# Kernel tuning notes

Measured on AMD Instinct MI355X. Metric: run time of the kernel, lower is better.

## Reference

```python
import jax, jax.numpy as jnp
import numpy as np

N_NODES = 50000
N_EDGES = 800000
IN_DIM = 6
HID = 256
OUT = 256
N_EXPERTS = 8
N_LAYERS = 2
N_GRAPHS = 64


def setup_inputs() -> dict:
    key = jax.random.key(0)
    ks = jax.random.split(key, 16)
    s = 0.05
    x = jax.random.normal(ks[0], (N_NODES, IN_DIM), dtype=jnp.float32)
    edge_index = jax.random.randint(ks[1], (2, N_EDGES), 0, N_NODES, dtype=jnp.int64)
    batch = jnp.sort(jax.random.randint(ks[2], (N_NODES,), 0, N_GRAPHS, dtype=jnp.int64))
    # shared encoder
    W_enc = jax.random.normal(ks[3], (IN_DIM, HID), jnp.float32) * s
    b_enc = jnp.zeros((HID,), jnp.float32)
    # router MLP: (HID+2) -> HID -> N_EXPERTS
    Wr1 = jax.random.normal(ks[4], (HID + 2, HID), jnp.float32) * s
    br1 = jnp.zeros((HID,), jnp.float32)
    Wr2 = jax.random.normal(ks[5], (HID, N_EXPERTS), jnp.float32) * s
    br2 = jnp.zeros((N_EXPERTS,), jnp.float32)
    # experts: 2 GraphConv layers each (self weight + neighbor weight + bias), stacked over experts
    Ws0 = jax.random.normal(ks[6], (N_EXPERTS, HID, HID), jnp.float32) * s
    Wn0 = jax.random.normal(ks[7], (N_EXPERTS, HID, HID), jnp.float32) * s
    b0 = jnp.zeros((N_EXPERTS, HID), jnp.float32)
    Ws1 = jax.random.normal(ks[8], (N_EXPERTS, HID, OUT), jnp.float32) * s
    Wn1 = jax.random.normal(ks[9], (N_EXPERTS, HID, OUT), jnp.float32) * s
    b1 = jnp.zeros((N_EXPERTS, OUT), jnp.float32)
    return dict(x=x, edge_index=edge_index, batch=batch, W_enc=W_enc, b_enc=b_enc,
                Wr1=Wr1, br1=br1, Wr2=Wr2, br2=br2,
                Ws0=Ws0, Wn0=Wn0, b0=b0, Ws1=Ws1, Wn1=Wn1, b1=b1)


def _graph_conv(h, src, dst, Ws, Wn, b):
    # PyG GraphConv: x' = x @ Ws + sum_{j in N(i)} x_j @ Wn + b
    msg = h[src] @ Wn                                   # [E, d_out]
    agg = jax.ops.segment_sum(msg, dst, num_segments=N_NODES)
    return h @ Ws + agg + b


def reference(x, edge_index, batch, W_enc, b_enc, Wr1, br1, Wr2, br2,
              Ws0, Wn0, b0, Ws1, Wn1, b1):
    src, dst = edge_index[0], edge_index[1]
    # shared encoder
    h = jax.nn.relu(x @ W_enc + b_enc)                  # [N, HID]
    # graph size features: per-graph node count and edge count, log-scaled, broadcast to nodes
    ones_n = jnp.ones((h.shape[0],), h.dtype)
    node_cnt = jax.ops.segment_sum(ones_n, batch, num_segments=N_GRAPHS)
    edge_cnt = jax.ops.segment_sum(jnp.ones((src.shape[0],), h.dtype), batch[src], num_segments=N_GRAPHS)
    size_feat = jnp.stack([jnp.log1p(node_cnt)[batch], jnp.log1p(edge_cnt)[batch]], axis=-1)  # [N, 2]
    # router -> top-1 expert index
    r = jax.nn.relu(jnp.concatenate([h, size_feat], axis=-1) @ Wr1 + br1)
    logits = r @ Wr2 + br2                              # [N, n_experts]
    idx = jnp.argmax(logits, axis=-1)                   # [N]
    # dense compute-all-experts, then gather by argmax (faithful to original)
    out = jnp.zeros((h.shape[0], Ws1.shape[-1]), h.dtype)
    for e in range(N_EXPERTS):
        z = jax.nn.relu(_graph_conv(h, src, dst, Ws0[e], Wn0[e], b0[e]))
        y_e = _graph_conv(z, src, dst, Ws1[e], Wn1[e], b1[e])   # [N, OUT]
        out = out + jnp.where((idx == e)[:, None], y_e, 0.0)
    return out
```

## Files before the change

### kernel.cpp

```cpp
#include <hip/hip_runtime.h>
#include <hip/hip_bf16.h>
#include <math.h>

#define NN 50000
#define NE 800000
#define NG 64
#define NEXP 8
#define ZC_CAP (3 * NN)

typedef __attribute__((ext_vector_type(8))) short bf16x8;
typedef __attribute__((ext_vector_type(4))) float f32x4;
typedef unsigned short ushort_t;

__device__ __forceinline__ unsigned short f2bf(float f) {
  union { float f; unsigned u; } x; x.f = f;
  unsigned r = x.u + 0x7fff + ((x.u >> 16) & 1);
  return (unsigned short)(r >> 16);
}
__device__ __forceinline__ float bf2f(unsigned short u) {
  union { unsigned u; float f; } x; x.u = ((unsigned)u) << 16; return x.f;
}

__device__ __forceinline__ void gld16(const void* g, void* l) {
  __builtin_amdgcn_global_load_lds(
      (const __attribute__((address_space(1))) unsigned int*)g,
      (__attribute__((address_space(3))) unsigned int*)l, 16, 0, 0);
}

__global__ __launch_bounds__(256) void k_encoder(
    const float* __restrict__ x, const float* __restrict__ W,
    const float* __restrict__ b, ushort_t* __restrict__ Xb,
    ushort_t* __restrict__ Xlo) {
  int i = blockIdx.x, n = threadIdx.x;
  float acc = b[n];
#pragma unroll
  for (int k = 0; k < 6; k++) acc = fmaf(x[i * 6 + k], W[k * 256 + n], acc);
  acc = fmaxf(acc, 0.f);
  unsigned short hb = f2bf(acc);
  Xb[(size_t)i * 512 + n] = hb;
  Xlo[(size_t)i * 256 + n] = f2bf(acc - bf2f(hb));
}

__global__ __launch_bounds__(256) void k_count_nodes(
    const int* __restrict__ batch, int* __restrict__ node_cnt) {
  __shared__ int bins[NG];
  int t = threadIdx.x;
  if (t < NG) bins[t] = 0;
  __syncthreads();
  for (int i = blockIdx.x * blockDim.x + t; i < NN; i += gridDim.x * blockDim.x)
    atomicAdd(&bins[batch[i]], 1);
  __syncthreads();
  if (t < NG) atomicAdd(&node_cnt[t], bins[t]);
}

__global__ __launch_bounds__(256) void k_count_edges(
    const int* __restrict__ ei, const int* __restrict__ batch,
    int* __restrict__ edge_cnt, int* __restrict__ deg) {
  __shared__ int bins[NG];
  int t = threadIdx.x;
  if (t < NG) bins[t] = 0;
  __syncthreads();
  for (int e = blockIdx.x * blockDim.x + t; e < NE; e += gridDim.x * blockDim.x) {
    int s = ei[e];
    int d = ei[NE + e];
    atomicAdd(&bins[batch[s]], 1);
    atomicAdd(&deg[d], 1);
  }
  __syncthreads();
  if (t < NG) atomicAdd(&edge_cnt[t], bins[t]);
}

__global__ __launch_bounds__(256) void k_sizefeat(
    const int* __restrict__ batch, const int* __restrict__ node_cnt,
    const int* __restrict__ edge_cnt, float* __restrict__ sf0,
    float* __restrict__ sf1) {
  int i = blockIdx.x * blockDim.x + threadIdx.x;
  if (i < NN) {
    int g = batch[i];
    sf0[i] = log1pf((float)node_cnt[g]);
    sf1[i] = log1pf((float)edge_cnt[g]);
  }
}

__global__ __launch_bounds__(1024) void k_scan(
    const int* __restrict__ deg, int* __restrict__ offs, int* __restrict__ cursor) {
  __shared__ int wsums[16];
  int t = threadIdx.x, lane = t & 63, wid = t >> 6;
  int carry = 0;
  for (int base = 0; base < NN; base += 1024) {
    int i = base + t;
    int v = (i < NN) ? deg[i] : 0;
    int x = v;
#pragma unroll
    for (int d = 1; d < 64; d <<= 1) {
      int y = __shfl_up(x, d, 64);
      if (lane >= d) x += y;
    }
    if (lane == 63) wsums[wid] = x;
    __syncthreads();
    if (wid == 0) {
      int s = (lane < 16) ? wsums[lane] : 0;
#pragma unroll
      for (int d = 1; d < 16; d <<= 1) {
        int y = __shfl_up(s, d, 64);
        if (lane >= d) s += y;
      }
      if (lane < 16) wsums[lane] = s;
    }
    __syncthreads();
    int wpre = (wid > 0) ? wsums[wid - 1] : 0;
    int excl = carry + wpre + x - v;
    if (i < NN) { offs[i] = excl; cursor[i] = excl; }
    int btot = wsums[15];
    __syncthreads();
    carry += btot;
  }
  if (t == 0) offs[NN] = carry;
}

__global__ __launch_bounds__(256) void k_fill_csr(
    const int* __restrict__ ei, int* __restrict__ cursor, int* __restrict__ edge_src) {
  int e = blockIdx.x * blockDim.x + threadIdx.x;
  if (e < NE) {
    int d = ei[NE + e];
    int pos = atomicAdd(&cursor[d], 1);
    edge_src[pos] = ei[e];
  }
}

__global__ __launch_bounds__(256) void k_agg_h2(
    const int* __restrict__ offs, const int* __restrict__ edge_src,
    ushort_t* __restrict__ Xb) {
  int wid = threadIdx.x >> 6, lane = threadIdx.x & 63;
  int half = lane >> 5, cl = lane & 31;
  int i = blockIdx.x * 4 + wid;
  if (i >= NN) return;
  int e0 = offs[i], e1 = offs[i + 1];
  float acc[8] = {};
  int k = e0;
  for (; k + 8 <= e1; k += 8) {
    int s0 = edge_src[k + half];
    int s1 = edge_src[k + 2 + half];
    int s2 = edge_src[k + 4 + half];
    int s3 = edge_src[k + 6 + half];
    bf16x8 v0 = *(const bf16x8*)&Xb[(size_t)s0 * 512 + cl * 8];
    bf16x8 v1 = *(const bf16x8*)&Xb[(size_t)s1 * 512 + cl * 8];
    bf16x8 v2 = *(const bf16x8*)&Xb[(size_t)s2 * 512 + cl * 8];
    bf16x8 v3 = *(const bf16x8*)&Xb[(size_t)s3 * 512 + cl * 8];
#pragma unroll
    for (int j = 0; j < 8; j++) acc[j] += bf2f((unsigned short)v0[j]);
#pragma unroll
    for (int j = 0; j < 8; j++) acc[j] += bf2f((unsigned short)v1[j]);
#pragma unroll
    for (int j = 0; j < 8; j++) acc[j] += bf2f((unsigned short)v2[j]);
#pragma unroll
    for (int j = 0; j < 8; j++) acc[j] += bf2f((unsigned short)v3[j]);
  }
  for (; k + 2 <= e1; k += 2) {
    int s0 = edge_src[k + half];
    bf16x8 v0 = *(const bf16x8*)&Xb[(size_t)s0 * 512 + cl * 8];
#pragma unroll
    for (int j = 0; j < 8; j++) acc[j] += bf2f((unsigned short)v0[j]);
  }
  if (k < e1 && half == 0) {
    int s0 = edge_src[k];
    bf16x8 v0 = *(const bf16x8*)&Xb[(size_t)s0 * 512 + cl * 8];
#pragma unroll
    for (int j = 0; j < 8; j++) acc[j] += bf2f((unsigned short)v0[j]);
  }
#pragma unroll
  for (int j = 0; j < 8; j++) acc[j] += __shfl_xor(acc[j], 32, 64);
  if (half == 0) {
    bf16x8 o;
#pragma unroll
    for (int j = 0; j < 8; j++) o[j] = (short)f2bf(acc[j]);
    *(bf16x8*)(&Xb[(size_t)i * 512 + 256 + cl * 8]) = o;
  }
}

__global__ __launch_bounds__(256) void k_prep_w(
    const float* __restrict__ Ws0, const float* __restrict__ Wn0,
    const float* __restrict__ Ws1, const float* __restrict__ Wn1,
    ushort_t* __restrict__ Wt1, ushort_t* __restrict__ Wt2) {
  __shared__ float tile[32][33];
  int z = blockIdx.z;
  int e = z & 7;
  const float* Ws = (z < 8) ? Ws0 : Ws1;
  const float* Wn = (z < 8) ? Wn0 : Wn1;
  ushort_t* Wt = (z < 8) ? Wt1 : Wt2;
  int kt = blockIdx.x;
  int nt = blockIdx.y;
  int tx = threadIdx.x & 31, ty = threadIdx.x >> 5;
  const float* src = (kt < 8) ? (Ws + e * 65536 + (kt * 32) * 256)
                              : (Wn + e * 65536 + ((kt - 8) * 32) * 256);
#pragma unroll
  for (int rr = 0; rr < 32; rr += 8) {
    int k = rr + ty;
    tile[k][tx] = src[k * 256 + nt * 32 + tx];
  }
  __syncthreads();
#pragma unroll
  for (int rr = 0; rr < 32; rr += 8) {
    int n = rr + ty;
    Wt[(size_t)e * 131072 + (nt * 32 + n) * 512 + kt * 32 + tx] = f2bf(tile[tx][n]);
  }
}

__global__ __launch_bounds__(256) void k_prep_wr1(
    const float* __restrict__ Wr1, ushort_t* __restrict__ Wr1t) {
  int k = blockIdx.x;
  int n = threadIdx.x;
  unsigned short v;
  if (k < 256) {
    v = f2bf(Wr1[k * 256 + n]);
  } else {
    float f = Wr1[(k - 256) * 256 + n];
    unsigned short h = f2bf(f);
    v = f2bf(f - bf2f(h));
  }
  Wr1t[(size_t)n * 512 + k] = v;
}

#define TIE_TAU 1e-4f
__global__ __launch_bounds__(256) void k_router_mfma(
    const ushort_t* __restrict__ Xb,
    const ushort_t* __restrict__ Xlo,
    const ushort_t* __restrict__ Wr1t,
    const float* __restrict__ Wr1, const float* __restrict__ br1,
    const float* __restrict__ Wr2, const float* __restrict__ sf0,
    const float* __restrict__ sf1, float* __restrict__ Lpart) {
  __shared__ ushort_t As[2][4096];
  __shared__ ushort_t Bs1[2][4096];
  __shared__ ushort_t Bs2[2][4096];
  __shared__ float Lsm[128][NEXP];
  int t = threadIdx.x;
  int w = t >> 6, lane = t & 63;
  int m0 = blockIdx.x * 128;
  int n0 = blockIdx.y * 128;
  int wm = w >> 1, wn = w & 1;
  int q16 = lane >> 4, c15 = lane & 15;
  for (int z = t; z < 128 * NEXP; z += 256) ((float*)Lsm)[z] = 0.f;

  auto STAGE = [&](int s, int kt) {
    int k0 = (kt & 7) * 32;
    bool hi = kt < 8;
#pragma unroll
    for (int i = 0; i < 2; i++) {
      int c = w * 128 + i * 64 + lane;
      int r = c >> 2, kc = c & 3;
      int kcs = kc ^ (r & 3);
      int gr = m0 + r; if (gr >= NN) gr = NN - 1;
      int dst = (w * 128 + i * 64) * 8;
      if (hi) {
        gld16(Xb + (size_t)gr * 512 + k0 + kcs * 8, (void*)&As[s][dst]);
        gld16(Wr1t + (size_t)(n0 + r) * 512 + k0 + kcs * 8, (void*)&Bs1[s][dst]);
        gld16(Wr1t + (size_t)(n0 + r) * 512 + 256 + k0 + kcs * 8, (void*)&Bs2[s][dst]);
      } else {
        gld16(Xlo + (size_t)gr * 256 + k0 + kcs * 8, (void*)&As[s][dst]);
        gld16(Wr1t + (size_t)(n0 + r) * 512 + k0 + kcs * 8, (void*)&Bs1[s][dst]);
      }
    }
  };

  f32x4 acc[4][4] = {};
  STAGE(0, 0);
  __syncthreads();
  for (int kt = 0; kt < 16; kt++) {
    int cur = kt & 1;
    if (kt < 15) STAGE(cur ^ 1, kt + 1);
    bf16x8 a[4], b1[4];
#pragma unroll
    for (int i = 0; i < 4; i++) {
      int ra = wm * 64 + i * 16 + c15;
      a[i] = *(const bf16x8*)&As[cur][ra * 32 + (q16 ^ (ra & 3)) * 8];
      int nb = wn * 64 + i * 16 + c15;
      b1[i] = *(const bf16x8*)&Bs1[cur][nb * 32 + (q16 ^ (nb & 3)) * 8];
    }
#pragma unroll
    for (int i = 0; i < 4; i++)
#pragma unroll
      for (int j = 0; j < 4; j++)
        acc[i][j] = __builtin_amdgcn_mfma_f32_16x16x32_bf16(a[i], b1[j], acc[i][j], 0, 0, 0);
    if (kt < 8) {
      bf16x8 b2[4];
#pragma unroll
      for (int i = 0; i < 4; i++) {
        int nb = wn * 64 + i * 16 + c15;
        b2[i] = *(const bf16x8*)&Bs2[cur][nb * 32 + (q16 ^ (nb & 3)) * 8];
      }
#pragma unroll
      for (int i = 0; i < 4; i++)
#pragma unroll
        for (int j = 0; j < 4; j++)
          acc[i][j] = __builtin_amdgcn_mfma_f32_16x16x32_bf16(a[i], b2[j], acc[i][j], 0, 0, 0);
    }
    __syncthreads();
  }

  float bb[4], w6[4], w7[4];
#pragma unroll
  for (int j = 0; j < 4; j++) {
    int col = n0 + wn * 64 + j * 16 + c15;
    bb[j] = br1[col];
    w6[j] = Wr1[65536 + col];
    w7[j] = Wr1[65792 + col];
  }
#pragma unroll
  for (int i = 0; i < 4; i++)
#pragma unroll
    for (int v = 0; v < 4; v++) {
      int row = m0 + wm * 64 + i * 16 + q16 * 4 + v;
      float s0v = (row < NN) ? sf0[row] : 0.f;
      float s1v = (row < NN) ? sf1[row] : 0.f;
#pragma unroll
      for (int j = 0; j < 4; j++)
        acc[i][j][v] = fmaxf(acc[i][j][v] + bb[j] + s0v * w6[j] + s1v * w7[j], 0.f);
    }
#pragma unroll
  for (int e = 0; e < NEXP; e++) {
    float wr2j[4];
#pragma unroll
    for (int j = 0; j < 4; j++)
      wr2j[j] = Wr2[(n0 + wn * 64 + j * 16 + c15) * 8 + e];
    float pe[4][4];
#pragma unroll
    for (int i = 0; i < 4; i++)
#pragma unroll
      for (int v = 0; v < 4; v++) {
        float s = acc[i][0][v] * wr2j[0];
        s = fmaf(acc[i][1][v], wr2j[1], s);
        s = fmaf(acc[i][2][v], wr2j[2], s);
        s = fmaf(acc[i][3][v], wr2j[3], s);
        pe[i][v] = s;
      }
#pragma unroll
    for (int d = 1; d < 16; d <<= 1)
#pragma unroll
      for (int i = 0; i < 4; i++)
#pragma unroll
        for (int v = 0; v < 4; v++)
          pe[i][v] += __shfl_xor(pe[i][v], d, 64);
    if (c15 == 0) {
#pragma unroll
      for (int i = 0; i < 4; i++)
#pragma unroll
        for (int v = 0; v < 4; v++)
          atomicAdd(&Lsm[wm * 64 + i * 16 + q16 * 4 + v][e], pe[i][v]);
    }
  }
  __syncthreads();
  for (int z = t; z < 128 * NEXP; z += 256) {
    int lr = z >> 3, e = z & 7;
    int row = m0 + lr;
    if (row < NN)
      Lpart[(size_t)blockIdx.y * (NN * 8) + (size_t)row * 8 + e] = Lsm[lr][e];
  }
}

__global__ __launch_bounds__(256) void k_argmax(
    const float* __restrict__ Lpart, const float* __restrict__ br2,
    int* __restrict__ idx, int* __restrict__ nfix, int* __restrict__ fixlist) {
  int i = blockIdx.x * 256 + threadIdx.x;
  if (i >= NN) return;
  float best = -1e30f, second = -1e30f; int bi = 0;
#pragma unroll
  for (int e = 0; e < NEXP; e++) {
    float v = br2[e] + Lpart[(size_t)i * 8 + e]
              + Lpart[(size_t)(NN * 8) + (size_t)i * 8 + e];
    if (v > best) { second = best; best = v; bi = e; }
    else if (v > second) second = v;
  }
  idx[i] = bi;
  if (best - second < TIE_TAU) {
    int p = atomicAdd(nfix, 1);
    fixlist[p] = i;
  }
}

__global__ __launch_bounds__(256) void k_fixup(
    const float* __restrict__ x, const float* __restrict__ W_enc,
    const float* __restrict__ b_enc, const float* __restrict__ Wr1,
    const float* __restrict__ br1, const float* __restrict__ Wr2,
    const float* __restrict__ br2, const float* __restrict__ sf0,
    const float* __restrict__ sf1, const int* __restrict__ fixlist,
    const int* __restrict__ nfix, int* __restrict__ idx) {
  __shared__ float hsh[256];
  __shared__ float lred[4][NEXP];
  int n = *nfix;
  int t = threadIdx.x, wid = t >> 6, lane = t & 63;
  for (int qq = blockIdx.x; qq < n; qq += gridDim.x) {
    int node = fixlist[qq];
    float hv = b_enc[t];
#pragma unroll
    for (int k = 0; k < 6; k++)
      hv = fmaf(x[node * 6 + k], W_enc[k * 256 + t], hv);
    hsh[t] = fmaxf(hv, 0.f);
    __syncthreads();
    float acc = br1[t] + sf0[node] * Wr1[65536 + t] + sf1[node] * Wr1[65792 + t];
    for (int k = 0; k < 256; k++)
      acc = fmaf(hsh[k], Wr1[k * 256 + t], acc);
    float r = fmaxf(acc, 0.f);
    float le[NEXP];
#pragma unroll
    for (int e = 0; e < NEXP; e++) le[e] = r * Wr2[t * 8 + e];
#pragma unroll
    for (int d = 32; d > 0; d >>= 1)
#pragma unroll
      for (int e = 0; e < NEXP; e++) le[e] += __shfl_xor(le[e], d, 64);
    if (lane == 0) {
#pragma unroll
      for (int e = 0; e < NEXP; e++) lred[wid][e] = le[e];
    }
    __syncthreads();
    if (t == 0) {
      float best = -1e30f; int bi = 0;
      for (int e = 0; e < NEXP; e++) {
        float v = lred[0][e] + lred[1][e] + lred[2][e] + lred[3][e] + br2[e];
        if (v > best) { best = v; bi = e; }
      }
      idx[node] = bi;
    }
    __syncthreads();
  }
}

__global__ __launch_bounds__(256) void k_ecnt(
    const int* __restrict__ idx, int* __restrict__ ecnt) {
  __shared__ int bins[NEXP];
  int t = threadIdx.x;
  if (t < NEXP) bins[t] = 0;
  __syncthreads();
  for (int i = blockIdx.x * 256 + t; i < NN; i += gridDim.x * 256)
    atomicAdd(&bins[idx[i]], 1);
  __syncthreads();
  if (t < NEXP) atomicAdd(&ecnt[t], bins[t]);
}

__global__ __launch_bounds__(256) void k_srcmask(
    const int* __restrict__ ei, const int* __restrict__ idx,
    unsigned int* __restrict__ mask) {
  int k = blockIdx.x * 256 + threadIdx.x;
  if (k < NE) {
    int s = ei[k], d = ei[NE + k];
    atomicOr(&mask[s], 1u << idx[d]);
  }
  if (k < NN) atomicOr(&mask[k], 1u << idx[k]);
}

__global__ __launch_bounds__(256) void k_scount(
    const unsigned int* __restrict__ mask, int* __restrict__ scnt) {
  __shared__ int bins[NEXP];
  int t = threadIdx.x;
  if (t < NEXP) bins[t] = 0;
  __syncthreads();
  for (int i = blockIdx.x * 256 + t; i < NN; i += gridDim.x * 256) {
    unsigned m = mask[i];
    while (m) { int b = __ffs(m) - 1; atomicAdd(&bins[b], 1); m &= m - 1; }
  }
  __syncthreads();
  if (t < NEXP) atomicAdd(&scnt[t], bins[t]);
}

__global__ void k_bucket_offs(const int* __restrict__ ecnt,
                              const int* __restrict__ scnt,
                              int* __restrict__ boff, int* __restrict__ bcur,
                              int* __restrict__ tstart,
                              int* __restrict__ soff, int* __restrict__ scur,
                              int* __restrict__ ltstart) {
  if (threadIdx.x == 0) {
    int s = 0, ts = 0, s2 = 0, lt = 0;
    for (int e = 0; e < NEXP; e++) {
      boff[e] = s; bcur[e] = s;
      tstart[e] = ts;
      ts += (ecnt[e] + 127) / 128;
      s += ecnt[e];
      soff[e] = s2; scur[e] = s2;
      ltstart[e] = lt;
      lt += (scnt[e] + 127) / 128;
      s2 += scnt[e];
    }
    boff[NEXP] = s;
    tstart[NEXP] = ts;
    soff[NEXP] = s2;
    ltstart[NEXP] = lt;
  }
}

#define BF_BLOCKS 64
__global__ __launch_bounds__(256) void k_bucket_fill2(
    const int* __restrict__ idx, int* __restrict__ bcur, int* __restrict__ nlist) {
  __shared__ int lcnt[NEXP];
  __shared__ int lbase[NEXP];
  int t = threadIdx.x;
  int chunk = (NN + BF_BLOCKS - 1) / BF_BLOCKS;
  int lo = blockIdx.x * chunk;
  int hi = lo + chunk; if (hi > NN) hi = NN;
  if (t < NEXP) lcnt[t] = 0;
  __syncthreads();
  for (int i = lo + t; i < hi; i += 256) atomicAdd(&lcnt[idx[i]], 1);
  __syncthreads();
  if (t < NEXP) lbase[t] = atomicAdd(&bcur[t], lcnt[t]);
  __syncthreads();
  if (t < NEXP) lcnt[t] = 0;
  __syncthreads();
  for (int i = lo + t; i < hi; i += 256) {
    int e = idx[i];
    int p = atomicAdd(&lcnt[e], 1);
    nlist[lbase[e] + p] = i;
  }
}

__global__ __launch_bounds__(256) void k_scompact(
    const unsigned int* __restrict__ mask, int* __restrict__ scur,
    int* __restrict__ slist, int* __restrict__ posmap) {
  __shared__ int lcnt[NEXP];
  __shared__ int lbase[NEXP];
  int t = threadIdx.x;
  int chunk = (NN + BF_BLOCKS - 1) / BF_BLOCKS;
  int lo = blockIdx.x * chunk;
  int hi = lo + chunk; if (hi > NN) hi = NN;
  if (t < NEXP) lcnt[t] = 0;
  __syncthreads();
  for (int i = lo + t; i < hi; i += 256) {
    unsigned m = mask[i];
    while (m) { int b = __ffs(m) - 1; atomicAdd(&lcnt[b], 1); m &= m - 1; }
  }
  __syncthreads();
  if (t < NEXP) lbase[t] = atomicAdd(&scur[t], lcnt[t]);
  __syncthreads();
  if (t < NEXP) lcnt[t] = 0;
  __syncthreads();
  for (int i = lo + t; i < hi; i += 256) {
    unsigned m = mask[i];
    while (m) {
      int b = __ffs(m) - 1;
      int p = atomicAdd(&lcnt[b], 1);
      int gp = lbase[b] + p;
      slist[gp] = i;
      posmap[(size_t)b * NN + i] = (gp < ZC_CAP) ? gp : 0;
      m &= m - 1;
    }
  }
}

#define MAXT1 (8 * 391 + 8)
__global__ __launch_bounds__(256) void k_layer1_all(
    const ushort_t* __restrict__ Abf,
    const ushort_t* __restrict__ Wt,
    const float* __restrict__ b0, const int* __restrict__ idx,
    const int* __restrict__ slist, const int* __restrict__ soff,
    const int* __restrict__ ltstart,
    ushort_t* __restrict__ Zc, ushort_t* __restrict__ A2) {
  int tx = blockIdx.x;
  int e = -1;
#pragma unroll
  for (int q = 0; q < NEXP; q++)
    if (tx >= ltstart[q] && tx < ltstart[q + 1]) e = q;
  if (e < 0) return;
  int tile = tx - ltstart[e];
  int base = soff[e];
  int cnt = soff[e + 1] - base;
  int m0 = tile * 128;
  __shared__ ushort_t As[2][4096];
  __shared__ ushort_t Bs[2][4096];
  __shared__ int rows[128];
  __shared__ int sidx[128];
  int t = threadIdx.x;
  if (t < 128) {
    int r = (m0 + t < cnt) ? slist[base + m0 + t] : -1;
    rows[t] = r;
    sidx[t] = (r >= 0) ? idx[r] : -1;
  }
  __syncthreads();
  int w = t >> 6, lane = t & 63;
  int n0 = blockIdx.y * 128;
  int wm = w >> 1, wn = w & 1;
  int q16 = lane >> 4, c15 = lane & 15;
  const ushort_t* Wb = Wt + (size_t)e * 131072;

  auto STAGE = [&](int s, int kt) {
    int k0 = kt * 32;
#pragma unroll
    for (int i = 0; i < 2; i++) {
      int c = w * 128 + i * 64 + lane;
      int r = c >> 2, kc = c & 3;
      int kcs = kc ^ (r & 3);
      int nd = rows[r]; if (nd < 0) nd = 0;
      int dst = (w * 128 + i * 64) * 8;
      gld16(Abf + (size_t)nd * 512 + k0 + kcs * 8, (void*)&As[s][dst]);
      gld16(Wb + (size_t)(n0 + r) * 512 + k0 + kcs * 8, (void*)&Bs[s][dst]);
    }
  };

  f32x4 acc[4][4] = {};
  STAGE(0, 0);
  __syncthreads();
  for (int kt = 0; kt < 16; kt++) {
    int cur = kt & 1;
    if (kt < 15) STAGE(cur ^ 1, kt + 1);
    bf16x8 a[4], b[4];
#pragma unroll
    for (int i = 0; i < 4; i++) {
      int ra = wm * 64 + i * 16 + c15;
      a[i] = *(const bf16x8*)&As[cur][ra * 32 + (q16 ^ (ra & 3)) * 8];
      int nb = wn * 64 + i * 16 + c15;
      b[i] = *(const bf16x8*)&Bs[cur][nb * 32 + (q16 ^ (nb & 3)) * 8];
    }
#pragma unroll
    for (int i = 0; i < 4; i++)
#pragma unroll
      for (int j = 0; j < 4; j++)
        acc[i][j] = __builtin_amdgcn_mfma_f32_16x16x32_bf16(a[i], b[j], acc[i][j], 0, 0, 0);
    __syncthreads();
  }
#pragma unroll
  for (int i = 0; i < 4; i++) {
#pragma unroll
    for (int j = 0; j < 4; j++) {
      int col = n0 + wn * 64 + j * 16 + c15;
      float bias = b0[e * 256 + col];
#pragma unroll
      for (int v = 0; v < 4; v++) {
        int lrow = wm * 64 + i * 16 + q16 * 4 + v;
        int node = rows[lrow];
        if (node >= 0) {
          unsigned short zb = f2bf(fmaxf(acc[i][j][v] + bias, 0.f));
          int sp = base + m0 + lrow;
          if (sp < ZC_CAP) Zc[(size_t)sp * 256 + col] = zb;
          if (sidx[lrow] == e) A2[(size_t)node * 512 + col] = zb;
        }
      }
    }
  }
}

__global__ __launch_bounds__(256) void k_agg_z_all(
    const ushort_t* __restrict__ Zc, const int* __restrict__ offs,
    const int* __restrict__ edge_src, const int* __restrict__ nlist,
    const int* __restrict__ boff, const int* __restrict__ posmap,
    ushort_t* __restrict__ A2) {
  int wid = threadIdx.x >> 6, lane = threadIdx.x & 63;
  int half = lane >> 5, cl = lane & 31;
  for (int b = blockIdx.x * 4 + wid; b < NN; b += gridDim.x * 4) {
    int e = 0;
#pragma unroll
    for (int q = 1; q < NEXP; q++)
      if (b >= boff[q]) e = q;
    int i = nlist[b];
    const int* pm = posmap + (size_t)e * NN;
    int e0 = offs[i], e1 = offs[i + 1];
    float acc[8] = {};
    int k = e0;
    for (; k + 8 <= e1; k += 8) {
      int s0 = edge_src[k + half];
      int s1 = edge_src[k + 2 + half];
      int s2 = edge_src[k + 4 + half];
      int s3 = edge_src[k + 6 + half];
      int p0 = pm[s0], p1 = pm[s1], p2 = pm[s2], p3 = pm[s3];
      bf16x8 v0 = *(const bf16x8*)&Zc[(size_t)p0 * 256 + cl * 8];
      bf16x8 v1 = *(const bf16x8*)&Zc[(size_t)p1 * 256 + cl * 8];
      bf16x8 v2 = *(const bf16x8*)&Zc[(size_t)p2 * 256 + cl * 8];
      bf16x8 v3 = *(const bf16x8*)&Zc[(size_t)p3 * 256 + cl * 8];
#pragma unroll
      for (int j = 0; j < 8; j++) acc[j] += bf2f((unsigned short)v0[j]);
#pragma unroll
      for (int j = 0; j < 8; j++) acc[j] += bf2f((unsigned short)v1[j]);
#pragma unroll
      for (int j = 0; j < 8; j++) acc[j] += bf2f((unsigned short)v2[j]);
#pragma unroll
      for (int j = 0; j < 8; j++) acc[j] += bf2f((unsigned short)v3[j]);
    }
    for (; k + 2 <= e1; k += 2) {
      int s0 = edge_src[k + half];
      int p0 = pm[s0];
      bf16x8 v0 = *(const bf16x8*)&Zc[(size_t)p0 * 256 + cl * 8];
#pragma unroll
      for (int j = 0; j < 8; j++) acc[j] += bf2f((unsigned short)v0[j]);
    }
    if (k < e1 && half == 0) {
      int s0 = edge_src[k];
      int p0 = pm[s0];
      bf16x8 v0 = *(const bf16x8*)&Zc[(size_t)p0 * 256 + cl * 8];
#pragma unroll
      for (int j = 0; j < 8; j++) acc[j] += bf2f((unsigned short)v0[j]);
    }
#pragma unroll
    for (int j = 0; j < 8; j++) acc[j] += __shfl_xor(acc[j], 32, 64);
    if (half == 0) {
      bf16x8 o;
#pragma unroll
      for (int j = 0; j < 8; j++) o[j] = (short)f2bf(acc[j]);
      *(bf16x8*)(&A2[(size_t)i * 512 + 256 + cl * 8]) = o;
    }
  }
}

#define MAXT2 (391 + NEXP)
__global__ __launch_bounds__(256) void k_layer2_mfma(
    const ushort_t* __restrict__ A2,
    const ushort_t* __restrict__ Wt,
    const float* __restrict__ b1, const int* __restrict__ nlist,
    const int* __restrict__ boff, const int* __restrict__ tstart,
    float* __restrict__ outp) {
  __shared__ ushort_t As[2][4096];
  __shared__ ushort_t Bs[2][4096];
  __shared__ int rows[128];
  int t = threadIdx.x;
  int tx = blockIdx.x;
  int e = -1;
#pragma unroll
  for (int q = 0; q < NEXP; q++)
    if (tx >= tstart[q] && tx < tstart[q + 1]) e = q;
  if (e < 0) return;
  int tile = tx - tstart[e];
  int base = boff[e];
  int cnt = boff[e + 1] - base;
  int m0 = tile * 128;
  if (t < 128) rows[t] = (m0 + t < cnt) ? nlist[base + m0 + t] : -1;
  __syncthreads();
  int w = t >> 6, lane = t & 63;
  int n0 = blockIdx.y * 128;
  int wm = w >> 1, wn = w & 1;
  int q16 = lane >> 4, c15 = lane & 15;
  const ushort_t* Wb = Wt + (size_t)e * 131072;

  auto STAGE = [&](int s, int kt) {
    int k0 = kt * 32;
#pragma unroll
    for (int i = 0; i < 2; i++) {
      int c = w * 128 + i * 64 + lane;
      int r = c >> 2, kc = c & 3;
      int kcs = kc ^ (r & 3);
      int nd = rows[r]; if (nd < 0) nd = 0;
      int dst = (w * 128 + i * 64) * 8;
      gld16(A2 + (size_t)nd * 512 + k0 + kcs * 8, (void*)&As[s][dst]);
      gld16(Wb + (size_t)(n0 + r) * 512 + k0 + kcs * 8, (void*)&Bs[s][dst]);
    }
  };

  f32x4 acc[4][4] = {};
  STAGE(0, 0);
  __syncthreads();
  for (int kt = 0; kt < 16; kt++) {
    int cur = kt & 1;
    if (kt < 15) STAGE(cur ^ 1, kt + 1);
    bf16x8 a[4], b[4];
#pragma unroll
    for (int i = 0; i < 4; i++) {
      int ra = wm * 64 + i * 16 + c15;
      a[i] = *(const bf16x8*)&As[cur][ra * 32 + (q16 ^ (ra & 3)) * 8];
      int nb = wn * 64 + i * 16 + c15;
      b[i] = *(const bf16x8*)&Bs[cur][nb * 32 + (q16 ^ (nb & 3)) * 8];
    }
#pragma unroll
    for (int i = 0; i < 4; i++)
#pragma unroll
      for (int j = 0; j < 4; j++)
        acc[i][j] = __builtin_amdgcn_mfma_f32_16x16x32_bf16(a[i], b[j], acc[i][j], 0, 0, 0);
    __syncthreads();
  }
#pragma unroll
  for (int i = 0; i < 4; i++) {
#pragma unroll
    for (int j = 0; j < 4; j++) {
      int col = n0 + wn * 64 + j * 16 + c15;
      float bias = b1[e * 256 + col];
#pragma unroll
      for (int v = 0; v < 4; v++) {
        int lrow = wm * 64 + i * 16 + q16 * 4 + v;
        int node = rows[lrow];
        if (node >= 0) outp[(size_t)node * 256 + col] = acc[i][j][v] + bias;
      }
    }
  }
}

static inline char* wsalloc(char*& p, size_t bytes) {
  char* r = p;
  p += (bytes + 255) & ~(size_t)255;
  return r;
}

extern "C" void kernel_launch(void* const* d_in, const int* in_sizes, int n_in,
                              void* d_out, int out_size, void* d_ws, size_t ws_size,
                              hipStream_t stream) {
  const float* x     = (const float*)d_in[0];
  const int*   ei    = (const int*)d_in[1];
  const int*   batch = (const int*)d_in[2];
  const float* W_enc = (const float*)d_in[3];
  const float* b_enc = (const float*)d_in[4];
  const float* Wr1   = (const float*)d_in[5];
  const float* br1   = (const float*)d_in[6];
  const float* Wr2   = (const float*)d_in[7];
  const float* br2   = (const float*)d_in[8];
  const float* Ws0   = (const float*)d_in[9];
  const float* Wn0   = (const float*)d_in[10];
  const float* b0    = (const float*)d_in[11];
  const float* Ws1   = (const float*)d_in[12];
  const float* Wn1   = (const float*)d_in[13];
  const float* b1    = (const float*)d_in[14];
  float* outp = (float*)d_out;

  char* p = (char*)d_ws;
  ushort_t* Xb   = (ushort_t*)wsalloc(p, (size_t)NN * 512 * 2);
  ushort_t* Zc   = (ushort_t*)wsalloc(p, (size_t)ZC_CAP * 256 * 2);
  ushort_t* A2   = (ushort_t*)wsalloc(p, (size_t)NN * 512 * 2);
  ushort_t* Xlo  = Zc;
  float*    Lpart= (float*)wsalloc(p, (size_t)2 * NN * 8 * 4);
  ushort_t* Wt1  = (ushort_t*)wsalloc(p, (size_t)NEXP * 256 * 512 * 2);
  ushort_t* Wt2  = (ushort_t*)wsalloc(p, (size_t)NEXP * 256 * 512 * 2);
  ushort_t* Wr1t = (ushort_t*)wsalloc(p, (size_t)256 * 512 * 2);
  int* edge_src  = (int*)wsalloc(p, (size_t)NE * 4);
  int* offs      = (int*)wsalloc(p, (size_t)(NN + 1) * 4);
  int* cursor    = (int*)wsalloc(p, (size_t)NN * 4);
  int* deg       = (int*)wsalloc(p, (size_t)NN * 4);
  int* idxb      = (int*)wsalloc(p, (size_t)NN * 4);
  float* sf0     = (float*)wsalloc(p, (size_t)NN * 4);
  float* sf1     = (float*)wsalloc(p, (size_t)NN * 4);
  int* nlist     = (int*)wsalloc(p, (size_t)NN * 4);
  int* fixlist   = (int*)wsalloc(p, (size_t)NN * 4);
  unsigned int* maskb = (unsigned int*)wsalloc(p, (size_t)NN * 4);
  int* slist     = (int*)wsalloc(p, (size_t)NN * NEXP * 4);
  int* posmap    = (int*)wsalloc(p, (size_t)NN * NEXP * 4);
  int* smallb    = (int*)wsalloc(p, 256 * 4);
  int* node_cnt = smallb;
  int* edge_cnt = smallb + 64;
  int* ecnt     = smallb + 128;
  int* boff     = smallb + 136;
  int* bcur     = smallb + 152;
  int* tstart   = smallb + 160;
  int* nfix     = smallb + 192;
  int* scnt     = smallb + 200;
  int* soff     = smallb + 208;
  int* scur     = smallb + 224;
  int* ltstart  = smallb + 232;

  hipMemsetAsync(deg, 0, (size_t)NN * 4, stream);
  hipMemsetAsync(smallb, 0, 256 * 4, stream);
  hipMemsetAsync(maskb, 0, (size_t)NN * 4, stream);

  k_encoder<<<NN, 256, 0, stream>>>(x, W_enc, b_enc, Xb, Xlo);
  k_count_nodes<<<64, 256, 0, stream>>>(batch, node_cnt);
  k_count_edges<<<128, 256, 0, stream>>>(ei, batch, edge_cnt, deg);
  k_sizefeat<<<(NN + 255) / 256, 256, 0, stream>>>(batch, node_cnt, edge_cnt, sf0, sf1);
  k_scan<<<1, 1024, 0, stream>>>(deg, offs, cursor);
  k_fill_csr<<<(NE + 255) / 256, 256, 0, stream>>>(ei, cursor, edge_src);
  k_agg_h2<<<(NN + 3) / 4, 256, 0, stream>>>(offs, edge_src, Xb);
  k_prep_w<<<dim3(16, 8, 16), 256, 0, stream>>>(Ws0, Wn0, Ws1, Wn1, Wt1, Wt2);
  k_prep_wr1<<<512, 256, 0, stream>>>(Wr1, Wr1t);
  k_router_mfma<<<dim3((NN + 127) / 128, 2), 256, 0, stream>>>(
      Xb, Xlo, Wr1t, Wr1, br1, Wr2, sf0, sf1, Lpart);
  k_argmax<<<(NN + 255) / 256, 256, 0, stream>>>(Lpart, br2, idxb, nfix, fixlist);
  k_fixup<<<256, 256, 0, stream>>>(x, W_enc, b_enc, Wr1, br1, Wr2, br2,
                                   sf0, sf1, fixlist, nfix, idxb);
  k_srcmask<<<(NE + 255) / 256, 256, 0, stream>>>(ei, idxb, maskb);
  k_ecnt<<<64, 256, 0, stream>>>(idxb, ecnt);
  k_scount<<<64, 256, 0, stream>>>(maskb, scnt);
  k_bucket_offs<<<1, 64, 0, stream>>>(ecnt, scnt, boff, bcur, tstart, soff, scur, ltstart);
  k_bucket_fill2<<<BF_BLOCKS, 256, 0, stream>>>(idxb, bcur, nlist);
  k_scompact<<<BF_BLOCKS, 256, 0, stream>>>(maskb, scur, slist, posmap);
  k_layer1_all<<<dim3(MAXT1, 2), 256, 0, stream>>>(
      Xb, Wt1, b0, idxb, slist, soff, ltstart, Zc, A2);
  k_agg_z_all<<<3125, 256, 0, stream>>>(Zc, offs, edge_src, nlist, boff, posmap, A2);
  k_layer2_mfma<<<dim3(MAXT2, 2), 256, 0, stream>>>(
      A2, Wt2, b1, nlist, boff, tstart, outp);
}
```

Before: 612.2 us.

## Use single-pass fp16 router GEMM instead of split bf16 and drop LDS swizzle

The router matmul previously emulated higher precision with split bf16 hi/lo operands over 16 k-steps with three-way MFMA. It now stores activations and router weights in fp16 and runs a single 8-step fp16 MFMA pass, widening the tie tolerance so more near-tie nodes are sent to the exact fixup path. The double-buffered staging in the router is replaced with a single buffer, and the XOR swizzle on LDS addressing is removed in the router and both expert GEMMs. This cuts router FLOPs and bytes, but risks LDS bank conflicts, lost load/compute overlap, and more fixup work or routing mismatches.

```diff
diff --git a/kernel.cpp b/kernel.cpp
--- a/kernel.cpp
+++ b/kernel.cpp
@@ -9,6 +9,7 @@
 #define ZC_CAP (3 * NN)
 
 typedef __attribute__((ext_vector_type(8))) short bf16x8;
+typedef __attribute__((ext_vector_type(8))) _Float16 f16x8;
 typedef __attribute__((ext_vector_type(4))) float f32x4;
 typedef unsigned short ushort_t;
 
@@ -30,15 +31,14 @@
 __global__ __launch_bounds__(256) void k_encoder(
     const float* __restrict__ x, const float* __restrict__ W,
     const float* __restrict__ b, ushort_t* __restrict__ Xb,
-    ushort_t* __restrict__ Xlo) {
+    _Float16* __restrict__ Xh16) {
   int i = blockIdx.x, n = threadIdx.x;
   float acc = b[n];
 #pragma unroll
   for (int k = 0; k < 6; k++) acc = fmaf(x[i * 6 + k], W[k * 256 + n], acc);
   acc = fmaxf(acc, 0.f);
-  unsigned short hb = f2bf(acc);
-  Xb[(size_t)i * 512 + n] = hb;
-  Xlo[(size_t)i * 256 + n] = f2bf(acc - bf2f(hb));
+  Xb[(size_t)i * 512 + n] = f2bf(acc);
+  Xh16[(size_t)i * 256 + n] = (_Float16)acc;
 }
 
 __global__ __launch_bounds__(256) void k_count_nodes(
@@ -206,32 +206,22 @@
   }
 }
 
-__global__ __launch_bounds__(256) void k_prep_wr1(
-    const float* __restrict__ Wr1, ushort_t* __restrict__ Wr1t) {
+__global__ __launch_bounds__(256) void k_prep_wr1h(
+    const float* __restrict__ Wr1, _Float16* __restrict__ Wr1h) {
   int k = blockIdx.x;
   int n = threadIdx.x;
-  unsigned short v;
-  if (k < 256) {
-    v = f2bf(Wr1[k * 256 + n]);
-  } else {
-    float f = Wr1[(k - 256) * 256 + n];
-    unsigned short h = f2bf(f);
-    v = f2bf(f - bf2f(h));
-  }
-  Wr1t[(size_t)n * 512 + k] = v;
-}
-
-#define TIE_TAU 1e-4f
+  Wr1h[(size_t)n * 256 + k] = (_Float16)Wr1[k * 256 + n];
+}
+
+#define TIE_TAU 2.5e-4f
 __global__ __launch_bounds__(256) void k_router_mfma(
-    const ushort_t* __restrict__ Xb,
-    const ushort_t* __restrict__ Xlo,
-    const ushort_t* __restrict__ Wr1t,
+    const _Float16* __restrict__ Xh16,
+    const _Float16* __restrict__ Wr1h,
     const float* __restrict__ Wr1, const float* __restrict__ br1,
     const float* __restrict__ Wr2, const float* __restrict__ sf0,
     const float* __restrict__ sf1, float* __restrict__ Lpart) {
-  __shared__ ushort_t As[2][4096];
-  __shared__ ushort_t Bs1[2][4096];
-  __shared__ ushort_t Bs2[2][4096];
+  __shared__ ushort_t As[4096];
+  __shared__ ushort_t Bs[4096];
   __shared__ float Lsm[128][NEXP];
   int t = threadIdx.x;
   int w = t >> 6, lane = t & 63;
@@ -241,59 +231,32 @@
   int q16 = lane >> 4, c15 = lane & 15;
   for (int z = t; z < 128 * NEXP; z += 256) ((float*)Lsm)[z] = 0.f;
 
-  auto STAGE = [&](int s, int kt) {
-    int k0 = (kt & 7) * 32;
-    bool hi = kt < 8;
+  f32x4 acc[4][4] = {};
+  for (int kt = 0; kt < 8; kt++) {
+    int k0 = kt * 32;
 #pragma unroll
     for (int i = 0; i < 2; i++) {
       int c = w * 128 + i * 64 + lane;
       int r = c >> 2, kc = c & 3;
-      int kcs = kc ^ (r & 3);
       int gr = m0 + r; if (gr >= NN) gr = NN - 1;
       int dst = (w * 128 + i * 64) * 8;
-      if (hi) {
-        gld16(Xb + (size_t)gr * 512 + k0 + kcs * 8, (void*)&As[s][dst]);
-        gld16(Wr1t + (size_t)(n0 + r) * 512 + k0 + kcs * 8, (void*)&Bs1[s][dst]);
-        gld16(Wr1t + (size_t)(n0 + r) * 512 + 256 + k0 + kcs * 8, (void*)&Bs2[s][dst]);
-      } else {
-        gld16(Xlo + (size_t)gr * 256 + k0 + kcs * 8, (void*)&As[s][dst]);
-        gld16(Wr1t + (size_t)(n0 + r) * 512 + k0 + kcs * 8, (void*)&Bs1[s][dst]);
-      }
-    }
-  };
-
-  f32x4 acc[4][4] = {};
-  STAGE(0, 0);
-  __syncthreads();
-  for (int kt = 0; kt < 16; kt++) {
-    int cur = kt & 1;
-    if (kt < 15) STAGE(cur ^ 1, kt + 1);
-    bf16x8 a[4], b1[4];
+      gld16(Xh16 + (size_t)gr * 256 + k0 + kc * 8, (void*)&As[dst]);
+      gld16(Wr1h + (size_t)(n0 + r) * 256 + k0 + kc * 8, (void*)&Bs[dst]);
+    }
+    __syncthreads();
+    f16x8 a[4], b[4];
 #pragma unroll
     for (int i = 0; i < 4; i++) {
       int ra = wm * 64 + i * 16 + c15;
-      a[i] = *(const bf16x8*)&As[cur][ra * 32 + (q16 ^ (ra & 3)) * 8];
+      a[i] = *(const f16x8*)&As[ra * 32 + q16 * 8];
       int nb = wn * 64 + i * 16 + c15;
-      b1[i] = *(const bf16x8*)&Bs1[cur][nb * 32 + (q16 ^ (nb & 3)) * 8];
+      b[i] = *(const f16x8*)&Bs[nb * 32 + q16 * 8];
     }
 #pragma unroll
     for (int i = 0; i < 4; i++)
 #pragma unroll
       for (int j = 0; j < 4; j++)
-        acc[i][j] = __builtin_amdgcn_mfma_f32_16x16x32_bf16(a[i], b1[j], acc[i][j], 0, 0, 0);
-    if (kt < 8) {
-      bf16x8 b2[4];
-#pragma unroll
-      for (int i = 0; i < 4; i++) {
-        int nb = wn * 64 + i * 16 + c15;
-        b2[i] = *(const bf16x8*)&Bs2[cur][nb * 32 + (q16 ^ (nb & 3)) * 8];
-      }
-#pragma unroll
-      for (int i = 0; i < 4; i++)
-#pragma unroll
-        for (int j = 0; j < 4; j++)
-          acc[i][j] = __builtin_amdgcn_mfma_f32_16x16x32_bf16(a[i], b2[j], acc[i][j], 0, 0, 0);
-    }
+        acc[i][j] = __builtin_amdgcn_mfma_f32_16x16x32_f16(a[i], b[j], acc[i][j], 0, 0, 0);
     __syncthreads();
   }
 
@@ -584,11 +547,10 @@
     for (int i = 0; i < 2; i++) {
       int c = w * 128 + i * 64 + lane;
       int r = c >> 2, kc = c & 3;
-      int kcs = kc ^ (r & 3);
       int nd = rows[r]; if (nd < 0) nd = 0;
       int dst = (w * 128 + i * 64) * 8;
-      gld16(Abf + (size_t)nd * 512 + k0 + kcs * 8, (void*)&As[s][dst]);
-      gld16(Wb + (size_t)(n0 + r) * 512 + k0 + kcs * 8, (void*)&Bs[s][dst]);
+      gld16(Abf + (size_t)nd * 512 + k0 + kc * 8, (void*)&As[s][dst]);
+      gld16(Wb + (size_t)(n0 + r) * 512 + k0 + kc * 8, (void*)&Bs[s][dst]);
     }
   };
 
@@ -602,9 +564,9 @@
 #pragma unroll
     for (int i = 0; i < 4; i++) {
       int ra = wm * 64 + i * 16 + c15;
-      a[i] = *(const bf16x8*)&As[cur][ra * 32 + (q16 ^ (ra & 3)) * 8];
+      a[i] = *(const bf16x8*)&As[cur][ra * 32 + q16 * 8];
       int nb = wn * 64 + i * 16 + c15;
-      b[i] = *(const bf16x8*)&Bs[cur][nb * 32 + (q16 ^ (nb & 3)) * 8];
+      b[i] = *(const bf16x8*)&Bs[cur][nb * 32 + q16 * 8];
     }
 #pragma unroll
     for (int i = 0; i < 4; i++)
@@ -730,11 +692,10 @@
     for (int i = 0; i < 2; i++) {
       int c = w * 128 + i * 64 + lane;
       int r = c >> 2, kc = c & 3;
-      int kcs = kc ^ (r & 3);
       int nd = rows[r]; if (nd < 0) nd = 0;
       int dst = (w * 128 + i * 64) * 8;
-      gld16(A2 + (size_t)nd * 512 + k0 + kcs * 8, (void*)&As[s][dst]);
-      gld16(Wb + (size_t)(n0 + r) * 512 + k0 + kcs * 8, (void*)&Bs[s][dst]);
+      gld16(A2 + (size_t)nd * 512 + k0 + kc * 8, (void*)&As[s][dst]);
+      gld16(Wb + (size_t)(n0 + r) * 512 + k0 + kc * 8, (void*)&Bs[s][dst]);
     }
   };
 
@@ -748,9 +709,9 @@
 #pragma unroll
     for (int i = 0; i < 4; i++) {
       int ra = wm * 64 + i * 16 + c15;
-      a[i] = *(const bf16x8*)&As[cur][ra * 32 + (q16 ^ (ra & 3)) * 8];
+      a[i] = *(const bf16x8*)&As[cur][ra * 32 + q16 * 8];
       int nb = wn * 64 + i * 16 + c15;
-      b[i] = *(const bf16x8*)&Bs[cur][nb * 32 + (q16 ^ (nb & 3)) * 8];
+      b[i] = *(const bf16x8*)&Bs[cur][nb * 32 + q16 * 8];
     }
 #pragma unroll
     for (int i = 0; i < 4; i++)
@@ -805,11 +766,11 @@
   ushort_t* Xb   = (ushort_t*)wsalloc(p, (size_t)NN * 512 * 2);
   ushort_t* Zc   = (ushort_t*)wsalloc(p, (size_t)ZC_CAP * 256 * 2);
   ushort_t* A2   = (ushort_t*)wsalloc(p, (size_t)NN * 512 * 2);
-  ushort_t* Xlo  = Zc;
+  _Float16* Xh16 = (_Float16*)Zc;
   float*    Lpart= (float*)wsalloc(p, (size_t)2 * NN * 8 * 4);
   ushort_t* Wt1  = (ushort_t*)wsalloc(p, (size_t)NEXP * 256 * 512 * 2);
   ushort_t* Wt2  = (ushort_t*)wsalloc(p, (size_t)NEXP * 256 * 512 * 2);
-  ushort_t* Wr1t = (ushort_t*)wsalloc(p, (size_t)256 * 512 * 2);
+  _Float16* Wr1h = (_Float16*)wsalloc(p, (size_t)256 * 256 * 2);
   int* edge_src  = (int*)wsalloc(p, (size_t)NE * 4);
   int* offs      = (int*)wsalloc(p, (size_t)(NN + 1) * 4);
   int* cursor    = (int*)wsalloc(p, (size_t)NN * 4);
@@ -839,7 +800,7 @@
   hipMemsetAsync(smallb, 0, 256 * 4, stream);
   hipMemsetAsync(maskb, 0, (size_t)NN * 4, stream);
 
-  k_encoder<<<NN, 256, 0, stream>>>(x, W_enc, b_enc, Xb, Xlo);
+  k_encoder<<<NN, 256, 0, stream>>>(x, W_enc, b_enc, Xb, Xh16);
   k_count_nodes<<<64, 256, 0, stream>>>(batch, node_cnt);
   k_count_edges<<<128, 256, 0, stream>>>(ei, batch, edge_cnt, deg);
   k_sizefeat<<<(NN + 255) / 256, 256, 0, stream>>>(batch, node_cnt, edge_cnt, sf0, sf1);
@@ -847,9 +808,9 @@
   k_fill_csr<<<(NE + 255) / 256, 256, 0, stream>>>(ei, cursor, edge_src);
   k_agg_h2<<<(NN + 3) / 4, 256, 0, stream>>>(offs, edge_src, Xb);
   k_prep_w<<<dim3(16, 8, 16), 256, 0, stream>>>(Ws0, Wn0, Ws1, Wn1, Wt1, Wt2);
-  k_prep_wr1<<<512, 256, 0, stream>>>(Wr1, Wr1t);
+  k_prep_wr1h<<<256, 256, 0, stream>>>(Wr1, Wr1h);
   k_router_mfma<<<dim3((NN + 127) / 128, 2), 256, 0, stream>>>(
-      Xb, Xlo, Wr1t, Wr1, br1, Wr2, sf0, sf1, Lpart);
+      Xh16, Wr1h, Wr1, br1, Wr2, sf0, sf1, Lpart);
   k_argmax<<<(NN + 255) / 256, 256, 0, stream>>>(Lpart, br2, idxb, nfix, fixlist);
   k_fixup<<<256, 256, 0, stream>>>(x, W_enc, b_enc, Wr1, br1, Wr2, br2,
                                    sf0, sf1, fixlist, nfix, idxb);
```

Result: faster. 588.0 us (-4.0%).
